# Kernel optimization log

Measured on AMD Instinct MI355X. Metric: run time of the kernel, lower is better.

## Reference

```python
import jax, jax.numpy as jnp
import numpy as np

NUM_WAVELETS = 64      # W
NUM_OUT_CH = 32        # W' (one 2-layer MLP per output channel)
HIDDEN_DIM = 128       # H


def setup_inputs() -> dict:
    key = jax.random.key(0)
    k_x, k_w1, k_b1, k_w2, k_b2 = jax.random.split(key, 5)
    N, C, W, H, O = 4096, 32, NUM_WAVELETS, HIDDEN_DIM, NUM_OUT_CH
    # torch nn.Linear default init: U(-1/sqrt(fan_in), 1/sqrt(fan_in))
    lim1 = 1.0 / np.sqrt(W)
    lim2 = 1.0 / np.sqrt(H)
    return {
        "scalar_inputs": jax.random.normal(k_x, (N, C, W), dtype=jnp.float32),
        # Stacked weights of the O independent MLPs:
        "W1": jax.random.uniform(k_w1, (O, H, W), jnp.float32, -lim1, lim1),
        "b1": jax.random.uniform(k_b1, (O, H), jnp.float32, -lim1, lim1),
        "W2": jax.random.uniform(k_w2, (O, H), jnp.float32, -lim2, lim2),  # Linear(H->1) weight per MLP
        "b2": jax.random.uniform(k_b2, (O,), jnp.float32, -lim2, lim2),
    }


def reference(scalar_inputs, W1, b1, W2, b2):
    # scalar_inputs: [N, C, W]; W1: [O, H, W]; b1: [O, H]; W2: [O, H]; b2: [O]
    N, C, W = scalar_inputs.shape
    x = scalar_inputs.reshape(N * C, W)                      # [NC, W]
    # Batched first Linear over all O MLPs at once (replaces the per-MLP loop)
    h = jax.nn.silu(jnp.einsum("nw,ohw->noh", x, W1) + b1)   # [NC, O, H]
    out = jnp.einsum("noh,oh->no", h, W2) + b2               # [NC, O]
    return out.reshape(N, C, -1)                             # [N, C, O]
```

## Files before the change

### kernel.cpp

```cpp
#include <hip/hip_runtime.h>

#define NC    131072
#define WDIM  64
#define ODIM  32
#define HDIM  128
#define LOG2E 1.4426950408889634f
#define LN2   0.6931471805599453f

typedef __attribute__((ext_vector_type(8))) short bf16x8;
typedef __attribute__((ext_vector_type(4))) float f32x4;
typedef __attribute__((ext_vector_type(4))) float flt4;
typedef __attribute__((ext_vector_type(2))) float f32x2;

__device__ __forceinline__ short f2bf(float f) {
    union { float f; unsigned u; } v; v.f = f;
    unsigned r = (v.u + 0x7FFFu + ((v.u >> 16) & 1u)) >> 16;
    return (short)r;
}

__global__ void prep_kernel(const float* __restrict__ W1, const float* __restrict__ b1,
                            const float* __restrict__ w2, short* __restrict__ w1f,
                            float* __restrict__ b1w2) {
    if (blockIdx.x < 128) {
        int tid  = blockIdx.x * 256 + threadIdx.x;
        int lane = tid & 63;
        int frag = (tid >> 6) & 15;
        int o    = tid >> 10;
        int t    = frag >> 1;
        int k2   = frag & 1;
        const float* src = W1 + ((size_t)(o * HDIM + t * 16 + (lane & 15)) * WDIM
                                 + k2 * 32 + (lane >> 4) * 8);
        bf16x8 v;
        #pragma unroll
        for (int i = 0; i < 8; ++i) v[i] = f2bf(src[i] * -LOG2E);
        *reinterpret_cast<bf16x8*>(w1f + (size_t)tid * 8) = v;
    } else {
        int idx = (blockIdx.x - 128) * 256 + threadIdx.x;
        int o = idx >> 8, j = idx & 255;
        b1w2[idx] = (j < 128) ? b1[o * HDIM + j] * -LOG2E
                              : w2[o * HDIM + (j - 128)] * -LN2;
    }
}

__device__ __forceinline__ void async16(void* lds_dst, const void* g_src) {
    __builtin_amdgcn_global_load_lds(
        (const __attribute__((address_space(1))) unsigned int*)g_src,
        (__attribute__((address_space(3))) unsigned int*)lds_dst,
        16, 0, 0);
}

#define BUFSH 8704
#define OHALF 16

__global__ __launch_bounds__(256, 4)
void swr_main(const float* __restrict__ x, const short* __restrict__ w1f,
              const float* __restrict__ b1w2, const float* __restrict__ b2,
              float* __restrict__ out)
{
    __shared__ short w1lds[2 * BUFSH];
    const int tid  = threadIdx.x;
    const int lane = tid & 63;
    const int wid  = tid >> 6;
    const int col  = lane & 15;
    const int kq   = lane >> 4;
    const int oh   = blockIdx.x & 1;
    const int rb   = blockIdx.x >> 1;
    const int obase = oh * OHALF;
    const size_t rowbase = (size_t)rb * 256 + (size_t)wid * 64;

    bf16x8 xf[4][2];
    #pragma unroll
    for (int s = 0; s < 4; ++s) {
        #pragma unroll
        for (int k2 = 0; k2 < 2; ++k2) {
            const float* p = x + (rowbase + s * 16 + col) * WDIM + k2 * 32 + kq * 8;
            flt4 lo = *reinterpret_cast<const flt4*>(p);
            flt4 hi = *reinterpret_cast<const flt4*>(p + 4);
            bf16x8 a;
            a[0] = f2bf(lo[0]); a[1] = f2bf(lo[1]); a[2] = f2bf(lo[2]); a[3] = f2bf(lo[3]);
            a[4] = f2bf(hi[0]); a[5] = f2bf(hi[1]); a[6] = f2bf(hi[2]); a[7] = f2bf(hi[3]);
            xf[s][k2] = a;
        }
    }

    #pragma unroll
    for (int f = 0; f < 4; ++f) {
        int frag = wid * 4 + f;
        async16(&w1lds[frag * 512], w1f + (size_t)obase * 8192 + frag * 512 + lane * 8);
    }
    if (wid == 0)
        async16(&w1lds[8192], b1w2 + (size_t)obase * 256 + lane * 4);
    __syncthreads();

    float* op[4];
    #pragma unroll
    for (int s = 0; s < 4; ++s) op[s] = out + (rowbase + s * 16 + col) * ODIM;
    float pu[4] = {0.f, 0.f, 0.f, 0.f};

    #pragma unroll 1
    for (int o = 0; o < OHALF; ++o) {
        const int oabs = obase + o;
        const short* cur = &w1lds[(o & 1) * BUFSH];

        if (o > 0 && lane < 16) {
            #pragma unroll
            for (int s = 0; s < 4; ++s) op[s][oabs - 1] = pu[s];
        }

        if (o + 1 < OHALF) {
            const short* g = w1f + (size_t)(oabs + 1) * 8192;
            short* nb = &w1lds[((o + 1) & 1) * BUFSH];
            #pragma unroll
            for (int f = 0; f < 4; ++f) {
                int frag = wid * 4 + f;
                async16(nb + frag * 512, g + frag * 512 + lane * 8);
            }
            if (wid == 0)
                async16(nb + 8192, b1w2 + (size_t)(oabs + 1) * 256 + lane * 4);
        }
        const float b2o = b2[oabs];
        const flt4* bwl = reinterpret_cast<const flt4*>(cur + 8192);

        f32x2 part[4][2];
        #pragma unroll
        for (int s = 0; s < 4; ++s)
            #pragma unroll
            for (int p = 0; p < 2; ++p) part[s][p] = (f32x2){0.f, 0.f};

        #pragma unroll
        for (int t = 0; t < 8; ++t) {
            flt4 b1c = bwl[t * 4 + kq];
            flt4 w2c = bwl[32 + t * 4 + kq];
            bf16x8 f0 = *reinterpret_cast<const bf16x8*>(cur + (t * 2 + 0) * 512 + lane * 8);
            bf16x8 f1 = *reinterpret_cast<const bf16x8*>(cur + (t * 2 + 1) * 512 + lane * 8);
            #pragma unroll
            for (int s = 0; s < 4; ++s) {
                f32x4 acc = __builtin_amdgcn_mfma_f32_16x16x32_bf16(
                                f0, xf[s][0], (f32x4){b1c[0], b1c[1], b1c[2], b1c[3]}, 0, 0, 0);
                acc = __builtin_amdgcn_mfma_f32_16x16x32_bf16(f1, xf[s][1], acc, 0, 0, 0);
                #pragma unroll
                for (int p = 0; p < 2; ++p) {
                    f32x2 m  = { acc[2 * p], acc[2 * p + 1] };
                    f32x2 wp = { w2c[2 * p], w2c[2 * p + 1] };
                    f32x2 mw = m * wp;
                    f32x2 e  = { __builtin_amdgcn_exp2f(m.x),
                                 __builtin_amdgcn_exp2f(m.y) };
                    f32x2 d  = e + (f32x2){1.f, 1.f};
                    f32x2 sg = { __builtin_amdgcn_rcpf(d.x),
                                 __builtin_amdgcn_rcpf(d.y) };
                    part[s][p] = __builtin_elementwise_fma(mw, sg, part[s][p]);
                }
            }
        }

        #pragma unroll
        for (int s = 0; s < 4; ++s) {
            f32x2 u2 = part[s][0] + part[s][1];
            float u = u2.x + u2.y;
            u += __shfl_xor(u, 16);
            u += __shfl_xor(u, 32);
            pu[s] = u + b2o;
        }
        __syncthreads();
    }
    if (lane < 16) {
        #pragma unroll
        for (int s = 0; s < 4; ++s) op[s][obase + OHALF - 1] = pu[s];
    }
}

extern "C" void kernel_launch(void* const* d_in, const int* in_sizes, int n_in,
                              void* d_out, int out_size, void* d_ws, size_t ws_size,
                              hipStream_t stream)
{
    const float* x  = (const float*)d_in[0];
    const float* W1 = (const float*)d_in[1];
    const float* b1 = (const float*)d_in[2];
    const float* w2 = (const float*)d_in[3];
    const float* b2 = (const float*)d_in[4];
    float* out = (float*)d_out;
    short* w1f  = (short*)d_ws;
    float* b1w2 = (float*)((char*)d_ws + 512 * 1024);

    hipLaunchKernelGGL(prep_kernel, dim3(160), dim3(256), 0, stream,
                       W1, b1, w2, w1f, b1w2);
    hipLaunchKernelGGL(swr_main, dim3(NC / 128), dim3(256), 0, stream,
                       x, w1f, b1w2, b2, out);
}
```

Before: 207.9 us.

## Share one reciprocal across four sigmoids, vectorize output stores, remap block order

```diff
diff --git a/kernel.cpp b/kernel.cpp
--- a/kernel.cpp
+++ b/kernel.cpp
@@ -63,8 +63,8 @@
     const int wid  = tid >> 6;
     const int col  = lane & 15;
     const int kq   = lane >> 4;
-    const int oh   = blockIdx.x & 1;
-    const int rb   = blockIdx.x >> 1;
+    const int oh   = blockIdx.x >> 9;
+    const int rb   = blockIdx.x & 511;
     const int obase = oh * OHALF;
     const size_t rowbase = (size_t)rb * 256 + (size_t)wid * 64;
 
@@ -94,78 +94,92 @@
 
     float* op[4];
     #pragma unroll
-    for (int s = 0; s < 4; ++s) op[s] = out + (rowbase + s * 16 + col) * ODIM;
-    float pu[4] = {0.f, 0.f, 0.f, 0.f};
+    for (int s = 0; s < 4; ++s)
+        op[s] = out + (rowbase + s * 16 + col) * ODIM + obase;
+    flt4 pu[4];
 
     #pragma unroll 1
-    for (int o = 0; o < OHALF; ++o) {
-        const int oabs = obase + o;
-        const short* cur = &w1lds[(o & 1) * BUFSH];
-
-        if (o > 0 && lane < 16) {
-            #pragma unroll
-            for (int s = 0; s < 4; ++s) op[s][oabs - 1] = pu[s];
+    for (int oc = 0; oc < 4; ++oc) {
+        if (oc > 0 && lane < 16) {
+            #pragma unroll
+            for (int s = 0; s < 4; ++s)
+                *reinterpret_cast<flt4*>(op[s] + (oc - 1) * 4) = pu[s];
         }
 
-        if (o + 1 < OHALF) {
-            const short* g = w1f + (size_t)(oabs + 1) * 8192;
-            short* nb = &w1lds[((o + 1) & 1) * BUFSH];
-            #pragma unroll
-            for (int f = 0; f < 4; ++f) {
-                int frag = wid * 4 + f;
-                async16(nb + frag * 512, g + frag * 512 + lane * 8);
+        #pragma unroll
+        for (int j = 0; j < 4; ++j) {
+            const int o = oc * 4 + j;
+            const int oabs = obase + o;
+            const short* cur = &w1lds[(j & 1) * BUFSH];
+
+            if (o + 1 < OHALF) {
+                const short* g = w1f + (size_t)(oabs + 1) * 8192;
+                short* nb = &w1lds[((j + 1) & 1) * BUFSH];
+                #pragma unroll
+                for (int f = 0; f < 4; ++f) {
+                    int frag = wid * 4 + f;
+                    async16(nb + frag * 512, g + frag * 512 + lane * 8);
+                }
+                if (wid == 0)
+                    async16(nb + 8192, b1w2 + (size_t)(oabs + 1) * 256 + lane * 4);
             }
-            if (wid == 0)
-                async16(nb + 8192, b1w2 + (size_t)(oabs + 1) * 256 + lane * 4);
-        }
-        const float b2o = b2[oabs];
-        const flt4* bwl = reinterpret_cast<const flt4*>(cur + 8192);
-
-        f32x2 part[4][2];
-        #pragma unroll
-        for (int s = 0; s < 4; ++s)
-            #pragma unroll
-            for (int p = 0; p < 2; ++p) part[s][p] = (f32x2){0.f, 0.f};
-
-        #pragma unroll
-        for (int t = 0; t < 8; ++t) {
-            flt4 b1c = bwl[t * 4 + kq];
-            flt4 w2c = bwl[32 + t * 4 + kq];
-            bf16x8 f0 = *reinterpret_cast<const bf16x8*>(cur + (t * 2 + 0) * 512 + lane * 8);
-            bf16x8 f1 = *reinterpret_cast<const bf16x8*>(cur + (t * 2 + 1) * 512 + lane * 8);
-            #pragma unroll
-            for (int s = 0; s < 4; ++s) {
-                f32x4 acc = __builtin_amdgcn_mfma_f32_16x16x32_bf16(
-                                f0, xf[s][0], (f32x4){b1c[0], b1c[1], b1c[2], b1c[3]}, 0, 0, 0);
-                acc = __builtin_amdgcn_mfma_f32_16x16x32_bf16(f1, xf[s][1], acc, 0, 0, 0);
+            const float b2o = b2[oabs];
+            const flt4* bwl = reinterpret_cast<const flt4*>(cur + 8192);
+
+            f32x2 part[4][2];
+            #pragma unroll
+            for (int s = 0; s < 4; ++s)
                 #pragma unroll
-                for (int p = 0; p < 2; ++p) {
-                    f32x2 m  = { acc[2 * p], acc[2 * p + 1] };
-                    f32x2 wp = { w2c[2 * p], w2c[2 * p + 1] };
-                    f32x2 mw = m * wp;
-                    f32x2 e  = { __builtin_amdgcn_exp2f(m.x),
-                                 __builtin_amdgcn_exp2f(m.y) };
-                    f32x2 d  = e + (f32x2){1.f, 1.f};
-                    f32x2 sg = { __builtin_amdgcn_rcpf(d.x),
-                                 __builtin_amdgcn_rcpf(d.y) };
-                    part[s][p] = __builtin_elementwise_fma(mw, sg, part[s][p]);
+                for (int p = 0; p < 2; ++p) part[s][p] = (f32x2){0.f, 0.f};
+
+            #pragma unroll
+            for (int t = 0; t < 8; ++t) {
+                flt4 b1c = bwl[t * 4 + kq];
+                flt4 w2c = bwl[32 + t * 4 + kq];
+                bf16x8 f0 = *reinterpret_cast<const bf16x8*>(cur + (t * 2 + 0) * 512 + lane * 8);
+                bf16x8 f1 = *reinterpret_cast<const bf16x8*>(cur + (t * 2 + 1) * 512 + lane * 8);
+                #pragma unroll
+                for (int s = 0; s < 4; ++s) {
+                    f32x4 acc = __builtin_amdgcn_mfma_f32_16x16x32_bf16(
+                                    f0, xf[s][0], (f32x4){b1c[0], b1c[1], b1c[2], b1c[3]}, 0, 0, 0);
+                    acc = __builtin_amdgcn_mfma_f32_16x16x32_bf16(f1, xf[s][1], acc, 0, 0, 0);
+                    f32x2 mA  = { acc[0], acc[1] };
+                    f32x2 mB  = { acc[2], acc[3] };
+                    f32x2 mwA = mA * (f32x2){ w2c[0], w2c[1] };
+                    f32x2 mwB = mB * (f32x2){ w2c[2], w2c[3] };
+                    f32x2 eA  = { __builtin_amdgcn_exp2f(mA.x),
+                                  __builtin_amdgcn_exp2f(mA.y) };
+                    f32x2 eB  = { __builtin_amdgcn_exp2f(mB.x),
+                                  __builtin_amdgcn_exp2f(mB.y) };
+                    f32x2 dA  = eA + (f32x2){1.f, 1.f};
+                    f32x2 dB  = eB + (f32x2){1.f, 1.f};
+                    float qA  = dA.x * dA.y;
+                    float qB  = dB.x * dB.y;
+                    float R   = __builtin_amdgcn_rcpf(qA * qB);
+                    float iqA = R * qB;
+                    float iqB = R * qA;
+                    f32x2 sA  = { iqA * dA.y, iqA * dA.x };
+                    f32x2 sB  = { iqB * dB.y, iqB * dB.x };
+                    part[s][0] = __builtin_elementwise_fma(mwA, sA, part[s][0]);
+                    part[s][1] = __builtin_elementwise_fma(mwB, sB, part[s][1]);
                 }
             }
+
+            #pragma unroll
+            for (int s = 0; s < 4; ++s) {
+                f32x2 u2 = part[s][0] + part[s][1];
+                float u = u2.x + u2.y;
+                u += __shfl_xor(u, 16);
+                u += __shfl_xor(u, 32);
+                pu[s][j] = u + b2o;
+            }
+            __syncthreads();
         }
-
-        #pragma unroll
-        for (int s = 0; s < 4; ++s) {
-            f32x2 u2 = part[s][0] + part[s][1];
-            float u = u2.x + u2.y;
-            u += __shfl_xor(u, 16);
-            u += __shfl_xor(u, 32);
-            pu[s] = u + b2o;
-        }
-        __syncthreads();
     }
     if (lane < 16) {
         #pragma unroll
-        for (int s = 0; s < 4; ++s) op[s][obase + OHALF - 1] = pu[s];
+        for (int s = 0; s < 4; ++s)
+            *reinterpret_cast<flt4*>(op[s] + 12) = pu[s];
     }
 }
 
@@ -184,6 +198,6 @@
 
     hipLaunchKernelGGL(prep_kernel, dim3(160), dim3(256), 0, stream,
                        W1, b1, w2, w1f, b1w2);
-    hipLaunchKernelGGL(swr_main, dim3(NC / 128), dim3(256), 0, stream,
+    hipLaunchKernelGGL(swr_main, dim3(1024), dim3(256), 0, stream,
                        x, w1f, b1w2, b2, out);
 }
```

After: 217.8 us. +4.8%, slower.
